# Kernel tuning notes

Measured on AMD Instinct MI355X. Metric: run time of the kernel, lower is better.

The kernel has to match this reference:

```python
import jax, jax.numpy as jnp
import numpy as np

NUM_CLUSTERS = 128
C = NUM_CLUSTERS + 1  # bincount minlength = number_clusters + 1
SOFTMAX_TEMP = 1.0


def setup_inputs() -> dict:
    key = jax.random.key(0)
    k1, k2, k3, k4 = jax.random.split(key, 4)
    B, N, D = 32, 4096, 64
    Bc = 4  # clusters batch dim; heads = B // Bc = 8
    return {
        "queries": jax.random.normal(k1, (B, N, D), dtype=jnp.float32),
        "keys": jax.random.normal(k2, (B, N, D), dtype=jnp.float32),
        "values": jax.random.normal(k3, (B, N, D), dtype=jnp.float32),
        "clusters": jax.random.randint(k4, (Bc, N), 0, C).astype(jnp.int64),
    }


def _segment_sum_batched(x, groups, num_segments):
    # x: [B, N, D], groups: [B, N] -> [B, num_segments, D]
    return jax.vmap(lambda xb, gb: jax.ops.segment_sum(xb, gb, num_segments=num_segments))(x, groups)


def reference(queries, keys, values, clusters):
    B, N, D = queries.shape
    Bc = clusters.shape[0]
    rep = B // Bc
    g = clusters.astype(jnp.int32)
    # per-cluster counts (bincount with minlength=C)
    counts = jax.vmap(lambda gb: jax.ops.segment_sum(jnp.ones((N,), jnp.float32), gb, num_segments=C))(g)
    # repeat assignments/counts across heads: torch .repeat(rep, 1) == tile on dim 0
    groups = jnp.tile(g, (rep, 1))          # [B, N]
    counts = jnp.tile(counts, (rep, 1))     # [B, C]
    w = jnp.where(counts > 0, 1.0 / counts, 0.0)  # 1/counts (guard empty clusters)

    Q_center = _segment_sum_batched(queries, groups, C) * w[..., None]  # [B, C, D]
    K_center = _segment_sum_batched(keys, groups, C) * w[..., None]
    V_center = _segment_sum_batched(values, groups, C) * w[..., None]

    QK = jnp.einsum('bqd,bkd->bqk', Q_center, K_center)  # [B, C, C]
    A = jax.nn.softmax(SOFTMAX_TEMP * QK, axis=-1)
    # weighted softmax: reweight by key-cluster counts, renormalize
    A = A * counts[:, None, :]
    A_full = A / A.sum(axis=-1, keepdims=True)

    V = jnp.einsum('bqk,bkd->bqd', A_full, V_center)  # [B, C, D]
    # Broadcast centers back to all cluster members (gather)
    out = jnp.take_along_axis(V, groups[..., None], axis=1)  # [B, N, D]
    return out, A_full[:, :, 0]
```

## Files before the change

### kernel.cpp

```cpp
#include <hip/hip_runtime.h>

#define B_ 32
#define N_ 4096
#define D_ 64
#define C_ 129
#define BC_ 4
#define CG_ 33
#define QROWS_ 17

__global__ __launch_bounds__(1024) void k_sort(const int* __restrict__ cl,
                                               float* __restrict__ counts,
                                               int* __restrict__ offsets,
                                               int* __restrict__ sidx) {
    __shared__ int cnt[C_];
    __shared__ int base[C_];
    __shared__ int cur[C_];
    int bc = blockIdx.x, tid = threadIdx.x;
    for (int i = tid; i < C_; i += 1024) { cnt[i] = 0; cur[i] = 0; }
    __syncthreads();
    const int4* g4 = (const int4*)(cl + bc * N_);
    for (int n = tid; n < N_ / 4; n += 1024) {
        int4 c4 = g4[n];
        atomicAdd(&cnt[c4.x], 1);
        atomicAdd(&cnt[c4.y], 1);
        atomicAdd(&cnt[c4.z], 1);
        atomicAdd(&cnt[c4.w], 1);
    }
    __syncthreads();
    if (tid < C_) {
        int acc = 0;
        for (int i = 0; i < tid; i++) acc += cnt[i];
        base[tid] = acc;
    }
    __syncthreads();
    for (int i = tid; i < C_; i += 1024) {
        counts[bc * C_ + i] = (float)cnt[i];
        offsets[bc * (C_ + 1) + i] = base[i];
    }
    if (tid == 0) offsets[bc * (C_ + 1) + C_] = N_;
    for (int n = tid; n < N_ / 4; n += 1024) {
        int4 c4 = g4[n];
        int n0 = n * 4;
        sidx[bc * N_ + base[c4.x] + atomicAdd(&cur[c4.x], 1)] = n0;
        sidx[bc * N_ + base[c4.y] + atomicAdd(&cur[c4.y], 1)] = n0 + 1;
        sidx[bc * N_ + base[c4.z] + atomicAdd(&cur[c4.z], 1)] = n0 + 2;
        sidx[bc * N_ + base[c4.w] + atomicAdd(&cur[c4.w], 1)] = n0 + 3;
    }
}

__global__ __launch_bounds__(256) void k_segsum4(const float* __restrict__ q,
                                                 const float* __restrict__ k,
                                                 const float* __restrict__ v,
                                                 const int* __restrict__ offsets,
                                                 const int* __restrict__ sidx,
                                                 float* __restrict__ sums) {
    int bid = blockIdx.x;
    int cg = bid % CG_;
    int b = bid / CG_;
    int wave = threadIdx.x >> 6, lane = threadIdx.x & 63;
    int c = cg * 4 + wave;
    if (c >= C_) return;
    int bc = b & 3;
    int start = offsets[bc * (C_ + 1) + c];
    int end = offsets[bc * (C_ + 1) + c + 1];
    int cnt = end - start;
    int sub = lane >> 4, d4 = lane & 15;

    const float4* q4 = (const float4*)(q + (size_t)b * N_ * D_);
    const float4* k4 = (const float4*)(k + (size_t)b * N_ * D_);
    const float4* v4 = (const float4*)(v + (size_t)b * N_ * D_);
    const int* si = sidx + bc * N_;

    float4 aq = make_float4(0.f, 0.f, 0.f, 0.f);
    float4 ak = make_float4(0.f, 0.f, 0.f, 0.f);
    float4 av = make_float4(0.f, 0.f, 0.f, 0.f);

    if (cnt > 0) {
        int last = end - 1;
        int ia = start + sub, ib = ia + 4, ic = ia + 8, id = ia + 12;
        int ra = si[min(ia, last)], rb = si[min(ib, last)];
        int rc = si[min(ic, last)], rd = si[min(id, last)];
        for (int i0 = start; i0 < end; i0 += 16) {
            int ca = ia, cb = ib, cc = ic, cd = id;
            int ua = ra, ub = rb, uc = rc, ud = rd;
            ia += 16; ib += 16; ic += 16; id += 16;
            if (i0 + 16 < end) {
                ra = si[min(ia, last)]; rb = si[min(ib, last)];
                rc = si[min(ic, last)]; rd = si[min(id, last)];
            }
            float ma = (ca < end) ? 1.f : 0.f;
            float mb = (cb < end) ? 1.f : 0.f;
            float mc = (cc < end) ? 1.f : 0.f;
            float md = (cd < end) ? 1.f : 0.f;
            float4 qa = q4[ua * 16 + d4], qb = q4[ub * 16 + d4];
            float4 qc = q4[uc * 16 + d4], qd = q4[ud * 16 + d4];
            float4 ka = k4[ua * 16 + d4], kb = k4[ub * 16 + d4];
            float4 kc = k4[uc * 16 + d4], kd = k4[ud * 16 + d4];
            float4 va = v4[ua * 16 + d4], vb = v4[ub * 16 + d4];
            float4 vc = v4[uc * 16 + d4], vd = v4[ud * 16 + d4];
            aq.x += ma * qa.x + mb * qb.x + mc * qc.x + md * qd.x;
            aq.y += ma * qa.y + mb * qb.y + mc * qc.y + md * qd.y;
            aq.z += ma * qa.z + mb * qb.z + mc * qc.z + md * qd.z;
            aq.w += ma * qa.w + mb * qb.w + mc * qc.w + md * qd.w;
            ak.x += ma * ka.x + mb * kb.x + mc * kc.x + md * kd.x;
            ak.y += ma * ka.y + mb * kb.y + mc * kc.y + md * kd.y;
            ak.z += ma * ka.z + mb * kb.z + mc * kc.z + md * kd.z;
            ak.w += ma * ka.w + mb * kb.w + mc * kc.w + md * kd.w;
            av.x += ma * va.x + mb * vb.x + mc * vc.x + md * vd.x;
            av.y += ma * va.y + mb * vb.y + mc * vc.y + md * vd.y;
            av.z += ma * va.z + mb * vb.z + mc * vc.z + md * vd.z;
            av.w += ma * va.w + mb * vb.w + mc * vc.w + md * vd.w;
        }
    }
#pragma unroll
    for (int off = 16; off <= 32; off <<= 1) {
        aq.x += __shfl_xor(aq.x, off, 64); aq.y += __shfl_xor(aq.y, off, 64);
        aq.z += __shfl_xor(aq.z, off, 64); aq.w += __shfl_xor(aq.w, off, 64);
        ak.x += __shfl_xor(ak.x, off, 64); ak.y += __shfl_xor(ak.y, off, 64);
        ak.z += __shfl_xor(ak.z, off, 64); ak.w += __shfl_xor(ak.w, off, 64);
        av.x += __shfl_xor(av.x, off, 64); av.y += __shfl_xor(av.y, off, 64);
        av.z += __shfl_xor(av.z, off, 64); av.w += __shfl_xor(av.w, off, 64);
    }
    if (sub == 0) {
        float w = (cnt > 0) ? 1.f / (float)cnt : 0.f;
        float4 oq = make_float4(aq.x * w, aq.y * w, aq.z * w, aq.w * w);
        float4 ok = make_float4(ak.x * w, ak.y * w, ak.z * w, ak.w * w);
        float4 ov = make_float4(av.x * w, av.y * w, av.z * w, av.w * w);
        ((float4*)(sums + (size_t)b * C_ * D_))[c * 16 + d4] = oq;
        ((float4*)(sums + ((size_t)B_ + b) * C_ * D_))[c * 16 + d4] = ok;
        ((float4*)(sums + ((size_t)2 * B_ + b) * C_ * D_))[c * 16 + d4] = ov;
    }
}

__global__ __launch_bounds__(256, 2) void k_attn(const float* __restrict__ sums,
                                                 const float* __restrict__ counts,
                                                 float* __restrict__ vout,
                                                 float* __restrict__ aout) {
    __shared__ float4 kc4[C_ * 17];
    __shared__ float4 vc4[C_ * 17];
    __shared__ float cnt_s[C_];
    __shared__ float arow[4][4][132];

    int b = blockIdx.x >> 3;
    int qg = blockIdx.x & 7;
    int q0 = qg * QROWS_;
    int qcnt = min(QROWS_, C_ - q0);
    int tid = threadIdx.x;

    for (int i = tid; i < C_; i += 256)
        cnt_s[i] = counts[(b & 3) * C_ + i];

    const float4* qsum4 = (const float4*)(sums + (size_t)b * C_ * D_);
    const float4* ksum4 = (const float4*)(sums + ((size_t)B_ + b) * C_ * D_);
    const float4* vsum4 = (const float4*)(sums + ((size_t)2 * B_ + b) * C_ * D_);

    for (int i = tid; i < C_ * 16; i += 256) {
        int c = i >> 4, d4 = i & 15;
        kc4[c * 17 + d4] = ksum4[i];
        vc4[c * 17 + d4] = vsum4[i];
    }
    __syncthreads();

    int wave = __builtin_amdgcn_readfirstlane(tid >> 6);
    int lane = tid & 63;

    for (int tt = wave; tt * 4 < qcnt; tt += 4) {
        int t4 = tt * 4;
        const float4* qp0 = qsum4 + (size_t)(q0 + min(t4 + 0, qcnt - 1)) * 16;
        const float4* qp1 = qsum4 + (size_t)(q0 + min(t4 + 1, qcnt - 1)) * 16;
        const float4* qp2 = qsum4 + (size_t)(q0 + min(t4 + 2, qcnt - 1)) * 16;
        const float4* qp3 = qsum4 + (size_t)(q0 + min(t4 + 3, qcnt - 1)) * 16;
        float s0[4] = {0, 0, 0, 0}, s1[4] = {0, 0, 0, 0}, s2[4] = {0, 0, 0, 0};
#pragma unroll 4
        for (int d4 = 0; d4 < 16; d4++) {
            float4 kv0 = kc4[lane * 17 + d4];
            float4 kv1 = kc4[(lane + 64) * 17 + d4];
            float4 kv2 = kc4[128 * 17 + d4];
            float4 qv0 = qp0[d4], qv1 = qp1[d4], qv2 = qp2[d4], qv3 = qp3[d4];
            s0[0] += qv0.x * kv0.x + qv0.y * kv0.y + qv0.z * kv0.z + qv0.w * kv0.w;
            s1[0] += qv0.x * kv1.x + qv0.y * kv1.y + qv0.z * kv1.z + qv0.w * kv1.w;
            s2[0] += qv0.x * kv2.x + qv0.y * kv2.y + qv0.z * kv2.z + qv0.w * kv2.w;
            s0[1] += qv1.x * kv0.x + qv1.y * kv0.y + qv1.z * kv0.z + qv1.w * kv0.w;
            s1[1] += qv1.x * kv1.x + qv1.y * kv1.y + qv1.z * kv1.z + qv1.w * kv1.w;
            s2[1] += qv1.x * kv2.x + qv1.y * kv2.y + qv1.z * kv2.z + qv1.w * kv2.w;
            s0[2] += qv2.x * kv0.x + qv2.y * kv0.y + qv2.z * kv0.z + qv2.w * kv0.w;
            s1[2] += qv2.x * kv1.x + qv2.y * kv1.y + qv2.z * kv1.z + qv2.w * kv1.w;
            s2[2] += qv2.x * kv2.x + qv2.y * kv2.y + qv2.z * kv2.z + qv2.w * kv2.w;
            s0[3] += qv3.x * kv0.x + qv3.y * kv0.y + qv3.z * kv0.z + qv3.w * kv0.w;
            s1[3] += qv3.x * kv1.x + qv3.y * kv1.y + qv3.z * kv1.z + qv3.w * kv1.w;
            s2[3] += qv3.x * kv2.x + qv3.y * kv2.y + qv3.z * kv2.z + qv3.w * kv2.w;
        }
#pragma unroll
        for (int r = 0; r < 4; r++) {
            if (t4 + r >= qcnt) break;
            int qrow = q0 + t4 + r;
            float m = fmaxf(s0[r], s1[r]);
            if (lane == 0) m = fmaxf(m, s2[r]);
            for (int off = 32; off > 0; off >>= 1)
                m = fmaxf(m, __shfl_xor(m, off, 64));
            float e0 = __expf(s0[r] - m) * cnt_s[lane];
            float e1 = __expf(s1[r] - m) * cnt_s[lane + 64];
            float e2 = (lane == 0) ? __expf(s2[r] - m) * cnt_s[128] : 0.f;
            float sum = e0 + e1 + e2;
            for (int off = 32; off > 0; off >>= 1)
                sum += __shfl_xor(sum, off, 64);
            float inv = 1.f / sum;
            float a0 = e0 * inv, a1 = e1 * inv;
            arow[wave][r][lane] = a0;
            arow[wave][r][64 + lane] = a1;
            if (lane == 0) {
                arow[wave][r][128] = e2 * inv;
                aout[b * C_ + qrow] = a0;
            }
        }
        __builtin_amdgcn_s_waitcnt(0);
        __builtin_amdgcn_sched_barrier(0);
        int rr = lane >> 4, d4 = lane & 15;
        const float4* ar4 = (const float4*)arow[wave][rr];
        float4 o = make_float4(0.f, 0.f, 0.f, 0.f);
        for (int k4 = 0; k4 < 32; k4++) {
            float4 a4 = ar4[k4];
            float4 v0 = vc4[(k4 * 4 + 0) * 17 + d4];
            float4 v1 = vc4[(k4 * 4 + 1) * 17 + d4];
            float4 v2 = vc4[(k4 * 4 + 2) * 17 + d4];
            float4 v3 = vc4[(k4 * 4 + 3) * 17 + d4];
            o.x += a4.x * v0.x + a4.y * v1.x + a4.z * v2.x + a4.w * v3.x;
            o.y += a4.x * v0.y + a4.y * v1.y + a4.z * v2.y + a4.w * v3.y;
            o.z += a4.x * v0.z + a4.y * v1.z + a4.z * v2.z + a4.w * v3.z;
            o.w += a4.x * v0.w + a4.y * v1.w + a4.z * v2.w + a4.w * v3.w;
        }
        {
            float a128 = arow[wave][rr][128];
            float4 vv = vc4[128 * 17 + d4];
            o.x += a128 * vv.x; o.y += a128 * vv.y;
            o.z += a128 * vv.z; o.w += a128 * vv.w;
        }
        if (t4 + rr < qcnt) {
            float4* dst = (float4*)(vout + ((size_t)b * C_ + (q0 + t4 + rr)) * D_);
            dst[d4] = o;
        }
    }
}

__global__ __launch_bounds__(256) void k_gather(const float* __restrict__ vout,
                                                const int* __restrict__ cl,
                                                float* __restrict__ out) {
    int idx = blockIdx.x * 256 + threadIdx.x;
    int d4 = idx & 15;
    int n = (idx >> 4) & (N_ - 1);
    int b = idx >> 16;
    int c = cl[(b & 3) * N_ + n];
    const float4* src = (const float4*)(vout + ((size_t)b * C_ + c) * D_);
    ((float4*)out)[idx] = src[d4];
}

extern "C" void kernel_launch(void* const* d_in, const int* in_sizes, int n_in,
                              void* d_out, int out_size, void* d_ws, size_t ws_size,
                              hipStream_t stream) {
    const float* q = (const float*)d_in[0];
    const float* k = (const float*)d_in[1];
    const float* v = (const float*)d_in[2];
    const int* cl = (const int*)d_in[3];
    float* out = (float*)d_out;
    float* aout = out + (size_t)B_ * N_ * D_;

    float* ws = (float*)d_ws;
    float* counts = ws;
    float* sums = ws + 1024;
    float* vout = sums + (size_t)3 * B_ * C_ * D_;
    int* offsets = (int*)(vout + (size_t)B_ * C_ * D_);
    int* sidx = offsets + 4 * (C_ + 1);

    k_sort<<<BC_, 1024, 0, stream>>>(cl, counts, offsets, sidx);
    k_segsum4<<<B_ * CG_, 256, 0, stream>>>(q, k, v, offsets, sidx, sums);
    k_attn<<<B_ * 8, 256, 0, stream>>>(sums, counts, vout, aout);
    k_gather<<<(B_ * N_ * 16) / 256, 256, 0, stream>>>(vout, cl, out);
}
```

Baseline: 168.1 us.

## Fuse sort, segment-sum, attention and scatter into one persistent kernel with grid barriers

```diff
diff --git a/kernel.cpp b/kernel.cpp
--- a/kernel.cpp
+++ b/kernel.cpp
@@ -5,253 +5,267 @@
 #define D_ 64
 #define C_ 129
 #define BC_ 4
-#define CG_ 33
 #define QROWS_ 17
-
-__global__ __launch_bounds__(1024) void k_sort(const int* __restrict__ cl,
+#define NBLK_ 256
+
+__device__ __forceinline__ void gbar(int* bar, int idx) {
+    __syncthreads();
+    if (threadIdx.x == 0) {
+        __hip_atomic_fetch_add(&bar[idx], 1, __ATOMIC_RELEASE, __HIP_MEMORY_SCOPE_AGENT);
+        int spins = 0;
+        while (__hip_atomic_load(&bar[idx], __ATOMIC_RELAXED, __HIP_MEMORY_SCOPE_AGENT) < NBLK_) {
+            __builtin_amdgcn_s_sleep(32);
+            if (++spins > (1 << 21)) break;
+        }
+        (void)__hip_atomic_load(&bar[idx], __ATOMIC_ACQUIRE, __HIP_MEMORY_SCOPE_AGENT);
+    }
+    __syncthreads();
+}
+
+__global__ __launch_bounds__(256) void k_fused(const float* __restrict__ q,
+                                               const float* __restrict__ k,
+                                               const float* __restrict__ v,
+                                               const int* __restrict__ cl,
                                                float* __restrict__ counts,
                                                int* __restrict__ offsets,
-                                               int* __restrict__ sidx) {
-    __shared__ int cnt[C_];
-    __shared__ int base[C_];
-    __shared__ int cur[C_];
-    int bc = blockIdx.x, tid = threadIdx.x;
-    for (int i = tid; i < C_; i += 1024) { cnt[i] = 0; cur[i] = 0; }
-    __syncthreads();
-    const int4* g4 = (const int4*)(cl + bc * N_);
-    for (int n = tid; n < N_ / 4; n += 1024) {
-        int4 c4 = g4[n];
-        atomicAdd(&cnt[c4.x], 1);
-        atomicAdd(&cnt[c4.y], 1);
-        atomicAdd(&cnt[c4.z], 1);
-        atomicAdd(&cnt[c4.w], 1);
-    }
-    __syncthreads();
-    if (tid < C_) {
-        int acc = 0;
-        for (int i = 0; i < tid; i++) acc += cnt[i];
-        base[tid] = acc;
-    }
-    __syncthreads();
-    for (int i = tid; i < C_; i += 1024) {
-        counts[bc * C_ + i] = (float)cnt[i];
-        offsets[bc * (C_ + 1) + i] = base[i];
-    }
-    if (tid == 0) offsets[bc * (C_ + 1) + C_] = N_;
-    for (int n = tid; n < N_ / 4; n += 1024) {
-        int4 c4 = g4[n];
-        int n0 = n * 4;
-        sidx[bc * N_ + base[c4.x] + atomicAdd(&cur[c4.x], 1)] = n0;
-        sidx[bc * N_ + base[c4.y] + atomicAdd(&cur[c4.y], 1)] = n0 + 1;
-        sidx[bc * N_ + base[c4.z] + atomicAdd(&cur[c4.z], 1)] = n0 + 2;
-        sidx[bc * N_ + base[c4.w] + atomicAdd(&cur[c4.w], 1)] = n0 + 3;
-    }
-}
-
-__global__ __launch_bounds__(256) void k_segsum4(const float* __restrict__ q,
-                                                 const float* __restrict__ k,
-                                                 const float* __restrict__ v,
-                                                 const int* __restrict__ offsets,
-                                                 const int* __restrict__ sidx,
-                                                 float* __restrict__ sums) {
-    int bid = blockIdx.x;
-    int cg = bid % CG_;
-    int b = bid / CG_;
-    int wave = threadIdx.x >> 6, lane = threadIdx.x & 63;
-    int c = cg * 4 + wave;
-    if (c >= C_) return;
-    int bc = b & 3;
-    int start = offsets[bc * (C_ + 1) + c];
-    int end = offsets[bc * (C_ + 1) + c + 1];
-    int cnt = end - start;
-    int sub = lane >> 4, d4 = lane & 15;
-
-    const float4* q4 = (const float4*)(q + (size_t)b * N_ * D_);
-    const float4* k4 = (const float4*)(k + (size_t)b * N_ * D_);
-    const float4* v4 = (const float4*)(v + (size_t)b * N_ * D_);
-    const int* si = sidx + bc * N_;
-
-    float4 aq = make_float4(0.f, 0.f, 0.f, 0.f);
-    float4 ak = make_float4(0.f, 0.f, 0.f, 0.f);
-    float4 av = make_float4(0.f, 0.f, 0.f, 0.f);
-
-    if (cnt > 0) {
-        int last = end - 1;
-        int ia = start + sub, ib = ia + 4, ic = ia + 8, id = ia + 12;
-        int ra = si[min(ia, last)], rb = si[min(ib, last)];
-        int rc = si[min(ic, last)], rd = si[min(id, last)];
-        for (int i0 = start; i0 < end; i0 += 16) {
-            int ca = ia, cb = ib, cc = ic, cd = id;
-            int ua = ra, ub = rb, uc = rc, ud = rd;
-            ia += 16; ib += 16; ic += 16; id += 16;
-            if (i0 + 16 < end) {
-                ra = si[min(ia, last)]; rb = si[min(ib, last)];
-                rc = si[min(ic, last)]; rd = si[min(id, last)];
-            }
-            float ma = (ca < end) ? 1.f : 0.f;
-            float mb = (cb < end) ? 1.f : 0.f;
-            float mc = (cc < end) ? 1.f : 0.f;
-            float md = (cd < end) ? 1.f : 0.f;
-            float4 qa = q4[ua * 16 + d4], qb = q4[ub * 16 + d4];
-            float4 qc = q4[uc * 16 + d4], qd = q4[ud * 16 + d4];
-            float4 ka = k4[ua * 16 + d4], kb = k4[ub * 16 + d4];
-            float4 kc = k4[uc * 16 + d4], kd = k4[ud * 16 + d4];
-            float4 va = v4[ua * 16 + d4], vb = v4[ub * 16 + d4];
-            float4 vc = v4[uc * 16 + d4], vd = v4[ud * 16 + d4];
-            aq.x += ma * qa.x + mb * qb.x + mc * qc.x + md * qd.x;
-            aq.y += ma * qa.y + mb * qb.y + mc * qc.y + md * qd.y;
-            aq.z += ma * qa.z + mb * qb.z + mc * qc.z + md * qd.z;
-            aq.w += ma * qa.w + mb * qb.w + mc * qc.w + md * qd.w;
-            ak.x += ma * ka.x + mb * kb.x + mc * kc.x + md * kd.x;
-            ak.y += ma * ka.y + mb * kb.y + mc * kc.y + md * kd.y;
-            ak.z += ma * ka.z + mb * kb.z + mc * kc.z + md * kd.z;
-            ak.w += ma * ka.w + mb * kb.w + mc * kc.w + md * kd.w;
-            av.x += ma * va.x + mb * vb.x + mc * vc.x + md * vd.x;
-            av.y += ma * va.y + mb * vb.y + mc * vc.y + md * vd.y;
-            av.z += ma * va.z + mb * vb.z + mc * vc.z + md * vd.z;
-            av.w += ma * va.w + mb * vb.w + mc * vc.w + md * vd.w;
-        }
-    }
-#pragma unroll
-    for (int off = 16; off <= 32; off <<= 1) {
-        aq.x += __shfl_xor(aq.x, off, 64); aq.y += __shfl_xor(aq.y, off, 64);
-        aq.z += __shfl_xor(aq.z, off, 64); aq.w += __shfl_xor(aq.w, off, 64);
-        ak.x += __shfl_xor(ak.x, off, 64); ak.y += __shfl_xor(ak.y, off, 64);
-        ak.z += __shfl_xor(ak.z, off, 64); ak.w += __shfl_xor(ak.w, off, 64);
-        av.x += __shfl_xor(av.x, off, 64); av.y += __shfl_xor(av.y, off, 64);
-        av.z += __shfl_xor(av.z, off, 64); av.w += __shfl_xor(av.w, off, 64);
-    }
-    if (sub == 0) {
-        float w = (cnt > 0) ? 1.f / (float)cnt : 0.f;
-        float4 oq = make_float4(aq.x * w, aq.y * w, aq.z * w, aq.w * w);
-        float4 ok = make_float4(ak.x * w, ak.y * w, ak.z * w, ak.w * w);
-        float4 ov = make_float4(av.x * w, av.y * w, av.z * w, av.w * w);
-        ((float4*)(sums + (size_t)b * C_ * D_))[c * 16 + d4] = oq;
-        ((float4*)(sums + ((size_t)B_ + b) * C_ * D_))[c * 16 + d4] = ok;
-        ((float4*)(sums + ((size_t)2 * B_ + b) * C_ * D_))[c * 16 + d4] = ov;
-    }
-}
-
-__global__ __launch_bounds__(256, 2) void k_attn(const float* __restrict__ sums,
-                                                 const float* __restrict__ counts,
-                                                 float* __restrict__ vout,
-                                                 float* __restrict__ aout) {
+                                               int* __restrict__ sidx,
+                                               float* __restrict__ sums,
+                                               int* __restrict__ bar,
+                                               float* __restrict__ out,
+                                               float* __restrict__ aout) {
     __shared__ float4 kc4[C_ * 17];
     __shared__ float4 vc4[C_ * 17];
     __shared__ float cnt_s[C_];
     __shared__ float arow[4][4][132];
-
-    int b = blockIdx.x >> 3;
-    int qg = blockIdx.x & 7;
-    int q0 = qg * QROWS_;
-    int qcnt = min(QROWS_, C_ - q0);
+    __shared__ int scnt[C_];
+    __shared__ int sbase[C_];
+    __shared__ int scur[C_];
+
     int tid = threadIdx.x;
-
-    for (int i = tid; i < C_; i += 256)
-        cnt_s[i] = counts[(b & 3) * C_ + i];
-
-    const float4* qsum4 = (const float4*)(sums + (size_t)b * C_ * D_);
-    const float4* ksum4 = (const float4*)(sums + ((size_t)B_ + b) * C_ * D_);
-    const float4* vsum4 = (const float4*)(sums + ((size_t)2 * B_ + b) * C_ * D_);
-
-    for (int i = tid; i < C_ * 16; i += 256) {
-        int c = i >> 4, d4 = i & 15;
-        kc4[c * 17 + d4] = ksum4[i];
-        vc4[c * 17 + d4] = vsum4[i];
-    }
-    __syncthreads();
-
-    int wave = __builtin_amdgcn_readfirstlane(tid >> 6);
-    int lane = tid & 63;
-
-    for (int tt = wave; tt * 4 < qcnt; tt += 4) {
-        int t4 = tt * 4;
-        const float4* qp0 = qsum4 + (size_t)(q0 + min(t4 + 0, qcnt - 1)) * 16;
-        const float4* qp1 = qsum4 + (size_t)(q0 + min(t4 + 1, qcnt - 1)) * 16;
-        const float4* qp2 = qsum4 + (size_t)(q0 + min(t4 + 2, qcnt - 1)) * 16;
-        const float4* qp3 = qsum4 + (size_t)(q0 + min(t4 + 3, qcnt - 1)) * 16;
-        float s0[4] = {0, 0, 0, 0}, s1[4] = {0, 0, 0, 0}, s2[4] = {0, 0, 0, 0};
+    int bid = blockIdx.x;
+    int wave = tid >> 6, lane = tid & 63;
+
+    if (bid < BC_) {
+        int bc = bid;
+        for (int i = tid; i < C_; i += 256) { scnt[i] = 0; scur[i] = 0; }
+        __syncthreads();
+        const int4* g4 = (const int4*)(cl + bc * N_);
+        for (int n = tid; n < N_ / 4; n += 256) {
+            int4 c4 = g4[n];
+            atomicAdd(&scnt[c4.x], 1);
+            atomicAdd(&scnt[c4.y], 1);
+            atomicAdd(&scnt[c4.z], 1);
+            atomicAdd(&scnt[c4.w], 1);
+        }
+        __syncthreads();
+        if (tid < C_) {
+            int acc = 0;
+            for (int i = 0; i < tid; i++) acc += scnt[i];
+            sbase[tid] = acc;
+        }
+        __syncthreads();
+        for (int i = tid; i < C_; i += 256) {
+            counts[bc * C_ + i] = (float)scnt[i];
+            offsets[bc * (C_ + 1) + i] = sbase[i];
+        }
+        if (tid == 0) offsets[bc * (C_ + 1) + C_] = N_;
+        for (int n = tid; n < N_ / 4; n += 256) {
+            int4 c4 = g4[n];
+            int n0 = n * 4;
+            sidx[bc * N_ + sbase[c4.x] + atomicAdd(&scur[c4.x], 1)] = n0;
+            sidx[bc * N_ + sbase[c4.y] + atomicAdd(&scur[c4.y], 1)] = n0 + 1;
+            sidx[bc * N_ + sbase[c4.z] + atomicAdd(&scur[c4.z], 1)] = n0 + 2;
+            sidx[bc * N_ + sbase[c4.w] + atomicAdd(&scur[c4.w], 1)] = n0 + 3;
+        }
+    }
+    gbar(bar, 0);
+
+    {
+        int sub = lane >> 4, d4 = lane & 15;
+        for (int t = bid * 4 + wave; t < B_ * C_; t += 1024) {
+            int b = t / C_;
+            int c = t - b * C_;
+            int bc = b & 3;
+            int start = offsets[bc * (C_ + 1) + c];
+            int end = offsets[bc * (C_ + 1) + c + 1];
+            int cnt = end - start;
+
+            const float4* q4 = (const float4*)(q + (size_t)b * N_ * D_);
+            const float4* k4 = (const float4*)(k + (size_t)b * N_ * D_);
+            const float4* v4 = (const float4*)(v + (size_t)b * N_ * D_);
+            const int* si = sidx + bc * N_;
+
+            float4 aq = make_float4(0.f, 0.f, 0.f, 0.f);
+            float4 ak = make_float4(0.f, 0.f, 0.f, 0.f);
+            float4 av = make_float4(0.f, 0.f, 0.f, 0.f);
+
+            if (cnt > 0) {
+                int last = end - 1;
+                int ia = start + sub, ib = ia + 4, ic = ia + 8, id = ia + 12;
+                int ra = si[min(ia, last)], rb = si[min(ib, last)];
+                int rc = si[min(ic, last)], rd = si[min(id, last)];
+                for (int i0 = start; i0 < end; i0 += 16) {
+                    int ca = ia, cb = ib, cc = ic, cd = id;
+                    int ua = ra, ub = rb, uc = rc, ud = rd;
+                    ia += 16; ib += 16; ic += 16; id += 16;
+                    if (i0 + 16 < end) {
+                        ra = si[min(ia, last)]; rb = si[min(ib, last)];
+                        rc = si[min(ic, last)]; rd = si[min(id, last)];
+                    }
+                    float ma = (ca < end) ? 1.f : 0.f;
+                    float mb = (cb < end) ? 1.f : 0.f;
+                    float mc = (cc < end) ? 1.f : 0.f;
+                    float md = (cd < end) ? 1.f : 0.f;
+                    float4 qa = q4[ua * 16 + d4], qb = q4[ub * 16 + d4];
+                    float4 qc = q4[uc * 16 + d4], qd = q4[ud * 16 + d4];
+                    float4 ka = k4[ua * 16 + d4], kb = k4[ub * 16 + d4];
+                    float4 kc = k4[uc * 16 + d4], kd = k4[ud * 16 + d4];
+                    float4 va = v4[ua * 16 + d4], vb = v4[ub * 16 + d4];
+                    float4 vc = v4[uc * 16 + d4], vd = v4[ud * 16 + d4];
+                    aq.x += ma * qa.x + mb * qb.x + mc * qc.x + md * qd.x;
+                    aq.y += ma * qa.y + mb * qb.y + mc * qc.y + md * qd.y;
+                    aq.z += ma * qa.z + mb * qb.z + mc * qc.z + md * qd.z;
+                    aq.w += ma * qa.w + mb * qb.w + mc * qc.w + md * qd.w;
+                    ak.x += ma * ka.x + mb * kb.x + mc * kc.x + md * kd.x;
+                    ak.y += ma * ka.y + mb * kb.y + mc * kc.y + md * kd.y;
+                    ak.z += ma * ka.z + mb * kb.z + mc * kc.z + md * kd.z;
+                    ak.w += ma * ka.w + mb * kb.w + mc * kc.w + md * kd.w;
+                    av.x += ma * va.x + mb * vb.x + mc * vc.x + md * vd.x;
+                    av.y += ma * va.y + mb * vb.y + mc * vc.y + md * vd.y;
+                    av.z += ma * va.z + mb * vb.z + mc * vc.z + md * vd.z;
+                    av.w += ma * va.w + mb * vb.w + mc * vc.w + md * vd.w;
+                }
+            }
+#pragma unroll
+            for (int off = 16; off <= 32; off <<= 1) {
+                aq.x += __shfl_xor(aq.x, off, 64); aq.y += __shfl_xor(aq.y, off, 64);
+                aq.z += __shfl_xor(aq.z, off, 64); aq.w += __shfl_xor(aq.w, off, 64);
+                ak.x += __shfl_xor(ak.x, off, 64); ak.y += __shfl_xor(ak.y, off, 64);
+                ak.z += __shfl_xor(ak.z, off, 64); ak.w += __shfl_xor(ak.w, off, 64);
+                av.x += __shfl_xor(av.x, off, 64); av.y += __shfl_xor(av.y, off, 64);
+                av.z += __shfl_xor(av.z, off, 64); av.w += __shfl_xor(av.w, off, 64);
+            }
+            if (sub == 0) {
+                float w = (cnt > 0) ? 1.f / (float)cnt : 0.f;
+                float4 oq = make_float4(aq.x * w, aq.y * w, aq.z * w, aq.w * w);
+                float4 ok = make_float4(ak.x * w, ak.y * w, ak.z * w, ak.w * w);
+                float4 ov = make_float4(av.x * w, av.y * w, av.z * w, av.w * w);
+                ((float4*)(sums + (size_t)b * C_ * D_))[c * 16 + d4] = oq;
+                ((float4*)(sums + ((size_t)B_ + b) * C_ * D_))[c * 16 + d4] = ok;
+                ((float4*)(sums + ((size_t)2 * B_ + b) * C_ * D_))[c * 16 + d4] = ov;
+            }
+        }
+    }
+    gbar(bar, 1);
+
+    {
+        int b = bid >> 3;
+        int qg = bid & 7;
+        int q0 = qg * QROWS_;
+        int qcnt = min(QROWS_, C_ - q0);
+        int bc = b & 3;
+
+        for (int i = tid; i < C_; i += 256)
+            cnt_s[i] = counts[bc * C_ + i];
+
+        const float4* qsum4 = (const float4*)(sums + (size_t)b * C_ * D_);
+        const float4* ksum4 = (const float4*)(sums + ((size_t)B_ + b) * C_ * D_);
+        const float4* vsum4 = (const float4*)(sums + ((size_t)2 * B_ + b) * C_ * D_);
+
+        for (int i = tid; i < C_ * 16; i += 256) {
+            int c = i >> 4, d4 = i & 15;
+            kc4[c * 17 + d4] = ksum4[i];
+            vc4[c * 17 + d4] = vsum4[i];
+        }
+        __syncthreads();
+
+        const int* si = sidx + bc * N_;
+        float4* ob = (float4*)(out + (size_t)b * N_ * D_);
+
+        int wv = __builtin_amdgcn_readfirstlane(wave);
+
+        for (int tt = wv; tt * 4 < qcnt; tt += 4) {
+            int t4 = tt * 4;
+            const float4* qp0 = qsum4 + (size_t)(q0 + min(t4 + 0, qcnt - 1)) * 16;
+            const float4* qp1 = qsum4 + (size_t)(q0 + min(t4 + 1, qcnt - 1)) * 16;
+            const float4* qp2 = qsum4 + (size_t)(q0 + min(t4 + 2, qcnt - 1)) * 16;
+            const float4* qp3 = qsum4 + (size_t)(q0 + min(t4 + 3, qcnt - 1)) * 16;
+            float s0[4] = {0, 0, 0, 0}, s1[4] = {0, 0, 0, 0}, s2[4] = {0, 0, 0, 0};
 #pragma unroll 4
-        for (int d4 = 0; d4 < 16; d4++) {
-            float4 kv0 = kc4[lane * 17 + d4];
-            float4 kv1 = kc4[(lane + 64) * 17 + d4];
-            float4 kv2 = kc4[128 * 17 + d4];
-            float4 qv0 = qp0[d4], qv1 = qp1[d4], qv2 = qp2[d4], qv3 = qp3[d4];
-            s0[0] += qv0.x * kv0.x + qv0.y * kv0.y + qv0.z * kv0.z + qv0.w * kv0.w;
-            s1[0] += qv0.x * kv1.x + qv0.y * kv1.y + qv0.z * kv1.z + qv0.w * kv1.w;
-            s2[0] += qv0.x * kv2.x + qv0.y * kv2.y + qv0.z * kv2.z + qv0.w * kv2.w;
-            s0[1] += qv1.x * kv0.x + qv1.y * kv0.y + qv1.z * kv0.z + qv1.w * kv0.w;
-            s1[1] += qv1.x * kv1.x + qv1.y * kv1.y + qv1.z * kv1.z + qv1.w * kv1.w;
-            s2[1] += qv1.x * kv2.x + qv1.y * kv2.y + qv1.z * kv2.z + qv1.w * kv2.w;
-            s0[2] += qv2.x * kv0.x + qv2.y * kv0.y + qv2.z * kv0.z + qv2.w * kv0.w;
-            s1[2] += qv2.x * kv1.x + qv2.y * kv1.y + qv2.z * kv1.z + qv2.w * kv1.w;
-            s2[2] += qv2.x * kv2.x + qv2.y * kv2.y + qv2.z * kv2.z + qv2.w * kv2.w;
-            s0[3] += qv3.x * kv0.x + qv3.y * kv0.y + qv3.z * kv0.z + qv3.w * kv0.w;
-            s1[3] += qv3.x * kv1.x + qv3.y * kv1.y + qv3.z * kv1.z + qv3.w * kv1.w;
-            s2[3] += qv3.x * kv2.x + qv3.y * kv2.y + qv3.z * kv2.z + qv3.w * kv2.w;
-        }
+            for (int d4 = 0; d4 < 16; d4++) {
+                float4 kv0 = kc4[lane * 17 + d4];
+                float4 kv1 = kc4[(lane + 64) * 17 + d4];
+                float4 kv2 = kc4[128 * 17 + d4];
+                float4 qv0 = qp0[d4], qv1 = qp1[d4], qv2 = qp2[d4], qv3 = qp3[d4];
+                s0[0] += qv0.x * kv0.x + qv0.y * kv0.y + qv0.z * kv0.z + qv0.w * kv0.w;
+                s1[0] += qv0.x * kv1.x + qv0.y * kv1.y + qv0.z * kv1.z + qv0.w * kv1.w;
+                s2[0] += qv0.x * kv2.x + qv0.y * kv2.y + qv0.z * kv2.z + qv0.w * kv2.w;
+                s0[1] += qv1.x * kv0.x + qv1.y * kv0.y + qv1.z * kv0.z + qv1.w * kv0.w;
+                s1[1] += qv1.x * kv1.x + qv1.y * kv1.y + qv1.z * kv1.z + qv1.w * kv1.w;
+                s2[1] += qv1.x * kv2.x + qv1.y * kv2.y + qv1.z * kv2.z + qv1.w * kv2.w;
+                s0[2] += qv2.x * kv0.x + qv2.y * kv0.y + qv2.z * kv0.z + qv2.w * kv0.w;
+                s1[2] += qv2.x * kv1.x + qv2.y * kv1.y + qv2.z * kv1.z + qv2.w * kv1.w;
+                s2[2] += qv2.x * kv2.x + qv2.y * kv2.y + qv2.z * kv2.z + qv2.w * kv2.w;
+                s0[3] += qv3.x * kv0.x + qv3.y * kv0.y + qv3.z * kv0.z + qv3.w * kv0.w;
+                s1[3] += qv3.x * kv1.x + qv3.y * kv1.y + qv3.z * kv1.z + qv3.w * kv1.w;
+                s2[3] += qv3.x * kv2.x + qv3.y * kv2.y + qv3.z * kv2.z + qv3.w * kv2.w;
+            }
 #pragma unroll
-        for (int r = 0; r < 4; r++) {
-            if (t4 + r >= qcnt) break;
-            int qrow = q0 + t4 + r;
-            float m = fmaxf(s0[r], s1[r]);
-            if (lane == 0) m = fmaxf(m, s2[r]);
-            for (int off = 32; off > 0; off >>= 1)
-                m = fmaxf(m, __shfl_xor(m, off, 64));
-            float e0 = __expf(s0[r] - m) * cnt_s[lane];
-            float e1 = __expf(s1[r] - m) * cnt_s[lane + 64];
-            float e2 = (lane == 0) ? __expf(s2[r] - m) * cnt_s[128] : 0.f;
-            float sum = e0 + e1 + e2;
-            for (int off = 32; off > 0; off >>= 1)
-                sum += __shfl_xor(sum, off, 64);
-            float inv = 1.f / sum;
-            float a0 = e0 * inv, a1 = e1 * inv;
-            arow[wave][r][lane] = a0;
-            arow[wave][r][64 + lane] = a1;
-            if (lane == 0) {
-                arow[wave][r][128] = e2 * inv;
-                aout[b * C_ + qrow] = a0;
-            }
-        }
-        __builtin_amdgcn_s_waitcnt(0);
-        __builtin_amdgcn_sched_barrier(0);
-        int rr = lane >> 4, d4 = lane & 15;
-        const float4* ar4 = (const float4*)arow[wave][rr];
-        float4 o = make_float4(0.f, 0.f, 0.f, 0.f);
-        for (int k4 = 0; k4 < 32; k4++) {
-            float4 a4 = ar4[k4];
-            float4 v0 = vc4[(k4 * 4 + 0) * 17 + d4];
-            float4 v1 = vc4[(k4 * 4 + 1) * 17 + d4];
-            float4 v2 = vc4[(k4 * 4 + 2) * 17 + d4];
-            float4 v3 = vc4[(k4 * 4 + 3) * 17 + d4];
-            o.x += a4.x * v0.x + a4.y * v1.x + a4.z * v2.x + a4.w * v3.x;
-            o.y += a4.x * v0.y + a4.y * v1.y + a4.z * v2.y + a4.w * v3.y;
-            o.z += a4.x * v0.z + a4.y * v1.z + a4.z * v2.z + a4.w * v3.z;
-            o.w += a4.x * v0.w + a4.y * v1.w + a4.z * v2.w + a4.w * v3.w;
-        }
-        {
-            float a128 = arow[wave][rr][128];
-            float4 vv = vc4[128 * 17 + d4];
-            o.x += a128 * vv.x; o.y += a128 * vv.y;
-            o.z += a128 * vv.z; o.w += a128 * vv.w;
-        }
-        if (t4 + rr < qcnt) {
-            float4* dst = (float4*)(vout + ((size_t)b * C_ + (q0 + t4 + rr)) * D_);
-            dst[d4] = o;
-        }
-    }
-}
-
-__global__ __launch_bounds__(256) void k_gather(const float* __restrict__ vout,
-                                                const int* __restrict__ cl,
-                                                float* __restrict__ out) {
-    int idx = blockIdx.x * 256 + threadIdx.x;
-    int d4 = idx & 15;
-    int n = (idx >> 4) & (N_ - 1);
-    int b = idx >> 16;
-    int c = cl[(b & 3) * N_ + n];
-    const float4* src = (const float4*)(vout + ((size_t)b * C_ + c) * D_);
-    ((float4*)out)[idx] = src[d4];
+            for (int r = 0; r < 4; r++) {
+                if (t4 + r >= qcnt) break;
+                int qrow = q0 + t4 + r;
+                float m = fmaxf(s0[r], s1[r]);
+                if (lane == 0) m = fmaxf(m, s2[r]);
+                for (int off = 32; off > 0; off >>= 1)
+                    m = fmaxf(m, __shfl_xor(m, off, 64));
+                float e0 = __expf(s0[r] - m) * cnt_s[lane];
+                float e1 = __expf(s1[r] - m) * cnt_s[lane + 64];
+                float e2 = (lane == 0) ? __expf(s2[r] - m) * cnt_s[128] : 0.f;
+                float sum = e0 + e1 + e2;
+                for (int off = 32; off > 0; off >>= 1)
+                    sum += __shfl_xor(sum, off, 64);
+                float inv = 1.f / sum;
+                float a0 = e0 * inv, a1 = e1 * inv;
+                arow[wave][r][lane] = a0;
+                arow[wave][r][64 + lane] = a1;
+                if (lane == 0) {
+                    arow[wave][r][128] = e2 * inv;
+                    aout[b * C_ + qrow] = a0;
+                }
+            }
+            __builtin_amdgcn_s_waitcnt(0);
+            __builtin_amdgcn_sched_barrier(0);
+            int rr = lane >> 4, d4 = lane & 15;
+            const float4* ar4 = (const float4*)arow[wave][rr];
+            float4 o = make_float4(0.f, 0.f, 0.f, 0.f);
+            for (int k4 = 0; k4 < 32; k4++) {
+                float4 a4 = ar4[k4];
+                float4 v0 = vc4[(k4 * 4 + 0) * 17 + d4];
+                float4 v1 = vc4[(k4 * 4 + 1) * 17 + d4];
+                float4 v2 = vc4[(k4 * 4 + 2) * 17 + d4];
+                float4 v3 = vc4[(k4 * 4 + 3) * 17 + d4];
+                o.x += a4.x * v0.x + a4.y * v1.x + a4.z * v2.x + a4.w * v3.x;
+                o.y += a4.x * v0.y + a4.y * v1.y + a4.z * v2.y + a4.w * v3.y;
+                o.z += a4.x * v0.z + a4.y * v1.z + a4.z * v2.z + a4.w * v3.z;
+                o.w += a4.x * v0.w + a4.y * v1.w + a4.z * v2.w + a4.w * v3.w;
+            }
+            {
+                float a128 = arow[wave][rr][128];
+                float4 vv = vc4[128 * 17 + d4];
+                o.x += a128 * vv.x; o.y += a128 * vv.y;
+                o.z += a128 * vv.z; o.w += a128 * vv.w;
+            }
+            if (t4 + rr < qcnt) {
+                int qrow = q0 + t4 + rr;
+                int s = offsets[bc * (C_ + 1) + qrow];
+                int e = offsets[bc * (C_ + 1) + qrow + 1];
+                for (int mm = s; mm < e; mm++) {
+                    int n = si[mm];
+                    ob[n * 16 + d4] = o;
+                }
+            }
+        }
+    }
 }
 
 extern "C" void kernel_launch(void* const* d_in, const int* in_sizes, int n_in,
@@ -267,12 +281,11 @@
     float* ws = (float*)d_ws;
     float* counts = ws;
     float* sums = ws + 1024;
-    float* vout = sums + (size_t)3 * B_ * C_ * D_;
-    int* offsets = (int*)(vout + (size_t)B_ * C_ * D_);
+    int* bar = (int*)(sums + (size_t)3 * B_ * C_ * D_);
+    int* offsets = bar + 64;
     int* sidx = offsets + 4 * (C_ + 1);
 
-    k_sort<<<BC_, 1024, 0, stream>>>(cl, counts, offsets, sidx);
-    k_segsum4<<<B_ * CG_, 256, 0, stream>>>(q, k, v, offsets, sidx, sums);
-    k_attn<<<B_ * 8, 256, 0, stream>>>(sums, counts, vout, aout);
-    k_gather<<<(B_ * N_ * 16) / 256, 256, 0, stream>>>(vout, cl, out);
+    hipMemsetAsync(bar, 0, 64 * sizeof(int), stream);
+    k_fused<<<NBLK_, 256, 0, stream>>>(q, k, v, cl, counts, offsets, sidx,
+                                       sums, bar, out, aout);
 }
```

New measurement: 191.4 us. 1.14x slower.

## Fuse gather into attention kernel by scattering center rows to cluster members

Applied to the files above, without the earlier changes.

```diff
diff --git a/kernel.cpp b/kernel.cpp
--- a/kernel.cpp
+++ b/kernel.cpp
@@ -132,10 +132,12 @@
     }
 }
 
-__global__ __launch_bounds__(256, 2) void k_attn(const float* __restrict__ sums,
-                                                 const float* __restrict__ counts,
-                                                 float* __restrict__ vout,
-                                                 float* __restrict__ aout) {
+__global__ __launch_bounds__(256, 2) void k_attn_sc(const float* __restrict__ sums,
+                                                    const float* __restrict__ counts,
+                                                    const int* __restrict__ offsets,
+                                                    const int* __restrict__ sidx,
+                                                    float* __restrict__ out,
+                                                    float* __restrict__ aout) {
     __shared__ float4 kc4[C_ * 17];
     __shared__ float4 vc4[C_ * 17];
     __shared__ float cnt_s[C_];
@@ -146,9 +148,10 @@
     int q0 = qg * QROWS_;
     int qcnt = min(QROWS_, C_ - q0);
     int tid = threadIdx.x;
+    int bc = b & 3;
 
     for (int i = tid; i < C_; i += 256)
-        cnt_s[i] = counts[(b & 3) * C_ + i];
+        cnt_s[i] = counts[bc * C_ + i];
 
     const float4* qsum4 = (const float4*)(sums + (size_t)b * C_ * D_);
     const float4* ksum4 = (const float4*)(sums + ((size_t)B_ + b) * C_ * D_);
@@ -160,6 +163,9 @@
         vc4[c * 17 + d4] = vsum4[i];
     }
     __syncthreads();
+
+    const int* si = sidx + bc * N_;
+    float4* ob = (float4*)(out + (size_t)b * N_ * D_);
 
     int wave = __builtin_amdgcn_readfirstlane(tid >> 6);
     int lane = tid & 63;
@@ -236,22 +242,15 @@
             o.z += a128 * vv.z; o.w += a128 * vv.w;
         }
         if (t4 + rr < qcnt) {
-            float4* dst = (float4*)(vout + ((size_t)b * C_ + (q0 + t4 + rr)) * D_);
-            dst[d4] = o;
-        }
-    }
-}
-
-__global__ __launch_bounds__(256) void k_gather(const float* __restrict__ vout,
-                                                const int* __restrict__ cl,
-                                                float* __restrict__ out) {
-    int idx = blockIdx.x * 256 + threadIdx.x;
-    int d4 = idx & 15;
-    int n = (idx >> 4) & (N_ - 1);
-    int b = idx >> 16;
-    int c = cl[(b & 3) * N_ + n];
-    const float4* src = (const float4*)(vout + ((size_t)b * C_ + c) * D_);
-    ((float4*)out)[idx] = src[d4];
+            int qrow = q0 + t4 + rr;
+            int s = offsets[bc * (C_ + 1) + qrow];
+            int e = offsets[bc * (C_ + 1) + qrow + 1];
+            for (int mm = s; mm < e; mm++) {
+                int n = si[mm];
+                ob[n * 16 + d4] = o;
+            }
+        }
+    }
 }
 
 extern "C" void kernel_launch(void* const* d_in, const int* in_sizes, int n_in,
@@ -267,12 +266,10 @@
     float* ws = (float*)d_ws;
     float* counts = ws;
     float* sums = ws + 1024;
-    float* vout = sums + (size_t)3 * B_ * C_ * D_;
-    int* offsets = (int*)(vout + (size_t)B_ * C_ * D_);
+    int* offsets = (int*)(sums + (size_t)3 * B_ * C_ * D_);
     int* sidx = offsets + 4 * (C_ + 1);
 
     k_sort<<<BC_, 1024, 0, stream>>>(cl, counts, offsets, sidx);
     k_segsum4<<<B_ * CG_, 256, 0, stream>>>(q, k, v, offsets, sidx, sums);
-    k_attn<<<B_ * 8, 256, 0, stream>>>(sums, counts, vout, aout);
-    k_gather<<<(B_ * N_ * 16) / 256, 256, 0, stream>>>(vout, cl, out);
-}
+    k_attn_sc<<<B_ * 8, 256, 0, stream>>>(sums, counts, offsets, sidx, out, aout);
+}
```

After: 171.0 us. About the same (+1.7%).
